# Performance work log

Measured on AMD Instinct MI355X. Metric: run time of the kernel, lower is better.

Reference implementation:

```python
import jax, jax.numpy as jnp
import numpy as np

N_NODES = 200000
N_EDGES = 3200000


def _gcn_prep(edge_index, n_nodes):
    # Add self loops (PyG GCNConv default) and compute symmetric normalization.
    loops = jnp.arange(n_nodes, dtype=edge_index.dtype)
    src = jnp.concatenate([edge_index[0], loops])
    dst = jnp.concatenate([edge_index[1], loops])
    deg = jax.ops.segment_sum(jnp.ones_like(dst, dtype=jnp.float32), dst,
                              num_segments=n_nodes)
    dinv = jnp.where(deg > 0, jax.lax.rsqrt(deg), 0.0)
    norm = dinv[src] * dinv[dst]  # [E+N]
    return src, dst, norm


def _gcn_conv(x, src, dst, norm, W, b, n_nodes):
    h = x @ W                                   # [N, out]
    msg = h[src] * norm[:, None]                # gather + scale, [E+N, out]
    out = jax.ops.segment_sum(msg, dst, num_segments=n_nodes)  # scatter-add
    return out + b


def setup_inputs() -> dict:
    key = jax.random.key(0)
    k = jax.random.split(key, 4)
    x = jax.random.normal(k[0], (N_NODES, 4), dtype=jnp.float32)
    edge_index = jax.random.randint(k[1], (2, N_EDGES), 0, N_NODES, dtype=jnp.int64)
    W1 = jax.random.normal(k[2], (4, 16), dtype=jnp.float32) * (1.0 / np.sqrt(4))
    b1 = jnp.zeros((16,), dtype=jnp.float32)
    W2 = jax.random.normal(k[3], (16, 1), dtype=jnp.float32) * (1.0 / np.sqrt(16))
    b2 = jnp.zeros((1,), dtype=jnp.float32)
    return {"x": x, "edge_index": edge_index, "W1": W1, "b1": b1,
            "W2": W2, "b2": b2}


def reference(x, edge_index, W1, b1, W2, b2):
    n = x.shape[0]
    src, dst, norm = _gcn_prep(edge_index, n)
    h = _gcn_conv(x, src, dst, norm, W1, b1, n)
    h = jax.nn.relu(h)
    out = _gcn_conv(h, src, dst, norm, W2, b2, n)
    return out
```

## Files before the change

### kernel.cpp

```cpp
#include <hip/hip_runtime.h>


#define BSE   512
#define CH    16384
#define NBW   512
#define SH    9
#define NB    391
#define FCAP  10752
#define BSB   512
#define RSTG  ((FCAP + BSB - 1) / BSB)
#define NOEDGE 0xFFFFFFFFu

__global__ void k_bin(const int* __restrict__ src, const int* __restrict__ dst,
                      int E, unsigned* __restrict__ gcur,
                      unsigned* __restrict__ epack) {
    __shared__ unsigned cnt[NB];
    __shared__ unsigned cur[NB];
    __shared__ unsigned basec[NB];
    int b = blockIdx.x, t = threadIdx.x;
    for (int i = t; i < NB; i += BSE) cnt[i] = 0;
    __syncthreads();
    int lo = b * CH, hi = min(E, lo + CH);
    int aligned = (hi - lo) & ~3;
    for (int i = lo + 4 * t; i + 3 < hi; i += 4 * BSE) {
        int4 d4 = *(const int4*)(dst + i);
        atomicAdd(&cnt[((unsigned)d4.x) >> SH], 1u);
        atomicAdd(&cnt[((unsigned)d4.y) >> SH], 1u);
        atomicAdd(&cnt[((unsigned)d4.z) >> SH], 1u);
        atomicAdd(&cnt[((unsigned)d4.w) >> SH], 1u);
    }
    for (int i = lo + aligned + t; i < hi; i += BSE)
        atomicAdd(&cnt[((unsigned)dst[i]) >> SH], 1u);
    __syncthreads();
    for (int i = t; i < NB; i += BSE) {
        unsigned c = cnt[i];
        unsigned pad = (c + 15u) & ~15u;
        unsigned ofs = pad ? atomicAdd(&gcur[i], pad) : 0u;
        unsigned base = (unsigned)i * FCAP + ofs;
        basec[i] = base;
        cur[i] = base;
    }
    __syncthreads();
    for (int i = lo + 4 * t; i + 3 < hi; i += 4 * BSE) {
        int4 d4 = *(const int4*)(dst + i);
        int4 s4 = *(const int4*)(src + i);
        unsigned k0 = ((unsigned)d4.x) >> SH, k1 = ((unsigned)d4.y) >> SH;
        unsigned k2 = ((unsigned)d4.z) >> SH, k3 = ((unsigned)d4.w) >> SH;
        unsigned p0 = atomicAdd(&cur[k0], 1u);
        unsigned p1 = atomicAdd(&cur[k1], 1u);
        unsigned p2 = atomicAdd(&cur[k2], 1u);
        unsigned p3 = atomicAdd(&cur[k3], 1u);
        if (p0 < (k0 + 1u) * FCAP) epack[p0] = ((unsigned)s4.x << SH) | (((unsigned)d4.x) & (NBW - 1u));
        if (p1 < (k1 + 1u) * FCAP) epack[p1] = ((unsigned)s4.y << SH) | (((unsigned)d4.y) & (NBW - 1u));
        if (p2 < (k2 + 1u) * FCAP) epack[p2] = ((unsigned)s4.z << SH) | (((unsigned)d4.z) & (NBW - 1u));
        if (p3 < (k3 + 1u) * FCAP) epack[p3] = ((unsigned)s4.w << SH) | (((unsigned)d4.w) & (NBW - 1u));
    }
    for (int i = lo + aligned + t; i < hi; i += BSE) {
        unsigned d = (unsigned)dst[i];
        unsigned k = d >> SH;
        unsigned pos = atomicAdd(&cur[k], 1u);
        if (pos < (k + 1u) * FCAP)
            epack[pos] = ((unsigned)src[i] << SH) | (d & (NBW - 1u));
    }
    __syncthreads();
    for (int i = t; i < NB; i += BSE) {
        unsigned end = basec[i] + ((cnt[i] + 15u) & ~15u);
        unsigned kend = ((unsigned)i + 1u) * FCAP;
        if (end > kend) end = kend;
        for (unsigned p = cur[i]; p < end; ++p) epack[p] = NOEDGE;
    }
}

__global__ void k_build(unsigned* __restrict__ epack, const unsigned* __restrict__ gcur,
                        const float* __restrict__ x,
                        unsigned* __restrict__ rowofs, unsigned* __restrict__ rowcnt,
                        float* __restrict__ x_scaled, int N) {
    __shared__ unsigned stage[FCAP];
    __shared__ unsigned cnt[BSB];
    __shared__ unsigned sc[BSB];
    __shared__ unsigned cur[BSB];
    int k = blockIdx.x, t = threadIdx.x;
    unsigned base = (unsigned)k * FCAP;
    int len = min((int)gcur[k], FCAP);
    for (int i = 4 * t; i + 3 < len; i += 4 * BSB)
        *(int4*)&stage[i] = *(const int4*)(epack + base + i);
    if (t < (len & 3)) stage[(len & ~3) + t] = epack[base + (len & ~3) + t];
    cnt[t] = 0;
    __syncthreads();
    for (int i = t; i < len; i += BSB) {
        unsigned p = stage[i];
        if (p != NOEDGE) atomicAdd(&cnt[p & (NBW - 1u)], 1u);
    }
    __syncthreads();
    unsigned c = cnt[t];
    sc[t] = c;
    __syncthreads();
    for (int off = 1; off < BSB; off <<= 1) {
        unsigned u = (t >= off) ? sc[t - off] : 0;
        __syncthreads();
        sc[t] += u;
        __syncthreads();
    }
    unsigned excl = sc[t] - c;
    cur[t] = excl;
    int node = k * NBW + t;
    if (node < N) {
        rowofs[node] = base + excl;
        rowcnt[node] = c;
        float di = rsqrtf((float)(c + 1));
        float4 xv = ((const float4*)x)[node];
        ((float4*)x_scaled)[node] = make_float4(xv.x * di, xv.y * di, xv.z * di, xv.w * di);
    }
    __syncthreads();
    int lenv = (int)sc[BSB - 1];
    unsigned r[RSTG];
    int nr = 0;
    for (int i = t; i < len; i += BSB) r[nr++] = stage[i];
    __syncthreads();
    for (int j = 0; j < nr; ++j) {
        unsigned p = r[j];
        if (p != NOEDGE) {
            unsigned pos = atomicAdd(&cur[p & (NBW - 1u)], 1u);
            stage[pos] = p >> SH;
        }
    }
    __syncthreads();
    for (int i = 4 * t; i + 3 < lenv; i += 4 * BSB)
        *(int4*)(epack + base + i) = *(const int4*)&stage[i];
    if (t < (lenv & 3)) epack[base + (lenv & ~3) + t] = stage[(lenv & ~3) + t];
}

__global__ void k_agg1(const unsigned* __restrict__ esorted, const unsigned* __restrict__ rowofs,
                       const unsigned* __restrict__ rowcnt,
                       const float* __restrict__ x_scaled,
                       const float* __restrict__ W1, const float* __restrict__ b1,
                       const float* __restrict__ W2,
                       float* __restrict__ z_scaled, int N) {
    int node = blockIdx.x * blockDim.x + threadIdx.x;
    if (node >= N) return;
    unsigned lo = rowofs[node], c = rowcnt[node], hi = lo + c;
    float di = rsqrtf((float)(c + 1));
    const float4* xs4 = (const float4*)x_scaled;
    float4 a0 = xs4[node];
    float4 a1 = make_float4(0.f, 0.f, 0.f, 0.f);
    float4 a2 = make_float4(0.f, 0.f, 0.f, 0.f);
    float4 a3 = make_float4(0.f, 0.f, 0.f, 0.f);
    unsigned i = lo;
    for (; i + 3 < hi; i += 4) {
        float4 v0 = xs4[esorted[i]],     v1 = xs4[esorted[i + 1]];
        float4 v2 = xs4[esorted[i + 2]], v3 = xs4[esorted[i + 3]];
        a0.x += v0.x; a0.y += v0.y; a0.z += v0.z; a0.w += v0.w;
        a1.x += v1.x; a1.y += v1.y; a1.z += v1.z; a1.w += v1.w;
        a2.x += v2.x; a2.y += v2.y; a2.z += v2.z; a2.w += v2.w;
        a3.x += v3.x; a3.y += v3.y; a3.z += v3.z; a3.w += v3.w;
    }
    for (; i < hi; ++i) {
        float4 v = xs4[esorted[i]];
        a0.x += v.x; a0.y += v.y; a0.z += v.z; a0.w += v.w;
    }
    float p0 = di * (a0.x + a1.x + a2.x + a3.x);
    float p1 = di * (a0.y + a1.y + a2.y + a3.y);
    float p2 = di * (a0.z + a1.z + a2.z + a3.z);
    float p3 = di * (a0.w + a1.w + a2.w + a3.w);
    float z = 0.0f;
    #pragma unroll
    for (int cc = 0; cc < 16; ++cc) {
        float h1 = p0 * W1[0 * 16 + cc] + p1 * W1[1 * 16 + cc]
                 + p2 * W1[2 * 16 + cc] + p3 * W1[3 * 16 + cc] + b1[cc];
        h1 = fmaxf(h1, 0.0f);
        z += h1 * W2[cc];
    }
    z_scaled[node] = z * di;
}

__global__ void k_agg2(const unsigned* __restrict__ esorted, const unsigned* __restrict__ rowofs,
                       const unsigned* __restrict__ rowcnt,
                       const float* __restrict__ z_scaled,
                       const float* __restrict__ b2, float* __restrict__ out, int N) {
    int node = blockIdx.x * blockDim.x + threadIdx.x;
    if (node >= N) return;
    unsigned lo = rowofs[node], c = rowcnt[node], hi = lo + c;
    float di = rsqrtf((float)(c + 1));
    float a0 = z_scaled[node], a1 = 0.f, a2 = 0.f, a3 = 0.f;
    unsigned i = lo;
    for (; i + 3 < hi; i += 4) {
        a0 += z_scaled[esorted[i]];
        a1 += z_scaled[esorted[i + 1]];
        a2 += z_scaled[esorted[i + 2]];
        a3 += z_scaled[esorted[i + 3]];
    }
    for (; i < hi; ++i) a0 += z_scaled[esorted[i]];
    out[node] = di * (a0 + a1 + a2 + a3) + b2[0];
}

extern "C" void kernel_launch(void* const* d_in, const int* in_sizes, int n_in,
                              void* d_out, int out_size, void* d_ws, size_t ws_size,
                              hipStream_t stream) {
    const float* x  = (const float*)d_in[0];
    const int*   ei = (const int*)d_in[1];
    const float* W1 = (const float*)d_in[2];
    const float* b1 = (const float*)d_in[3];
    const float* W2 = (const float*)d_in[4];
    const float* b2 = (const float*)d_in[5];

    const int N = in_sizes[0] / 4;
    const int E = in_sizes[1] / 2;
    const int* src = ei;
    const int* dst = ei + E;
    const int NA = (E + CH - 1) / CH;

    char* ws = (char*)d_ws;
    unsigned* gcur      = (unsigned*)ws;  ws += 4096;
    unsigned* epack     = (unsigned*)ws;  ws += (size_t)NB * FCAP * 4;
    unsigned* rowofs    = (unsigned*)ws;  ws += (size_t)N * 4;
    unsigned* rowcnt    = (unsigned*)ws;  ws += (size_t)N * 4;
    float*    x_scaled  = (float*)ws;     ws += (size_t)N * 4 * 4;
    float*    z_scaled  = (float*)ws;     ws += (size_t)N * 4;
    float* out = (float*)d_out;

    hipMemsetAsync(gcur, 0, NB * sizeof(unsigned), stream);
    k_bin  <<<NA, BSE, 0, stream>>>(src, dst, E, gcur, epack);
    k_build<<<NB, BSB, 0, stream>>>(epack, gcur, x, rowofs, rowcnt, x_scaled, N);
    k_agg1 <<<(N + 255) / 256, 256, 0, stream>>>(epack, rowofs, rowcnt, x_scaled,
                                                 W1, b1, W2, z_scaled, N);
    k_agg2 <<<(N + 255) / 256, 256, 0, stream>>>(epack, rowofs, rowcnt, z_scaled,
                                                 b2, out, N);
}
```

Before: 172.4 us.

## Fuse binning, CSR build and both aggregations into one cooperative kernel

Replaces the four kernel launches with a single cooperative kernel of one block per 512-node bucket, separated by grid syncs. The sorted edge list stays in shared memory, so the write-back of sorted indices and the rowofs/rowcnt arrays go away, and both aggregation passes read neighbor ids from LDS. The cost is a grid of only about 391 blocks, each with roughly 50KB of shared memory, doing the binning with smaller chunks, plus three grid-wide barriers. Degree-skewed buckets may leave blocks idle during aggregation.

```diff
diff --git a/kernel.cpp b/kernel.cpp
--- a/kernel.cpp
+++ b/kernel.cpp
@@ -1,167 +1,161 @@
 #include <hip/hip_runtime.h>
-
-
-#define BSE   512
-#define CH    16384
-#define NBW   512
-#define SH    9
-#define NB    391
-#define FCAP  10752
-#define BSB   512
-#define RSTG  ((FCAP + BSB - 1) / BSB)
+#include <hip/hip_cooperative_groups.h>
+
+namespace cg = cooperative_groups;
+
+#define BS     512
+#define NBW    512
+#define SH     9
+#define CH2    8192
+#define FCAP   12608
+#define RSTG   ((FCAP + BS - 1) / BS)
 #define NOEDGE 0xFFFFFFFFu
 
-__global__ void k_bin(const int* __restrict__ src, const int* __restrict__ dst,
-                      int E, unsigned* __restrict__ gcur,
-                      unsigned* __restrict__ epack) {
-    __shared__ unsigned cnt[NB];
-    __shared__ unsigned cur[NB];
-    __shared__ unsigned basec[NB];
-    int b = blockIdx.x, t = threadIdx.x;
-    for (int i = t; i < NB; i += BSE) cnt[i] = 0;
-    __syncthreads();
-    int lo = b * CH, hi = min(E, lo + CH);
-    int aligned = (hi - lo) & ~3;
-    for (int i = lo + 4 * t; i + 3 < hi; i += 4 * BSE) {
-        int4 d4 = *(const int4*)(dst + i);
-        atomicAdd(&cnt[((unsigned)d4.x) >> SH], 1u);
-        atomicAdd(&cnt[((unsigned)d4.y) >> SH], 1u);
-        atomicAdd(&cnt[((unsigned)d4.z) >> SH], 1u);
-        atomicAdd(&cnt[((unsigned)d4.w) >> SH], 1u);
-    }
-    for (int i = lo + aligned + t; i < hi; i += BSE)
-        atomicAdd(&cnt[((unsigned)dst[i]) >> SH], 1u);
-    __syncthreads();
-    for (int i = t; i < NB; i += BSE) {
-        unsigned c = cnt[i];
-        unsigned pad = (c + 15u) & ~15u;
-        unsigned ofs = pad ? atomicAdd(&gcur[i], pad) : 0u;
-        unsigned base = (unsigned)i * FCAP + ofs;
-        basec[i] = base;
-        cur[i] = base;
-    }
-    __syncthreads();
-    for (int i = lo + 4 * t; i + 3 < hi; i += 4 * BSE) {
-        int4 d4 = *(const int4*)(dst + i);
-        int4 s4 = *(const int4*)(src + i);
-        unsigned k0 = ((unsigned)d4.x) >> SH, k1 = ((unsigned)d4.y) >> SH;
-        unsigned k2 = ((unsigned)d4.z) >> SH, k3 = ((unsigned)d4.w) >> SH;
-        unsigned p0 = atomicAdd(&cur[k0], 1u);
-        unsigned p1 = atomicAdd(&cur[k1], 1u);
-        unsigned p2 = atomicAdd(&cur[k2], 1u);
-        unsigned p3 = atomicAdd(&cur[k3], 1u);
-        if (p0 < (k0 + 1u) * FCAP) epack[p0] = ((unsigned)s4.x << SH) | (((unsigned)d4.x) & (NBW - 1u));
-        if (p1 < (k1 + 1u) * FCAP) epack[p1] = ((unsigned)s4.y << SH) | (((unsigned)d4.y) & (NBW - 1u));
-        if (p2 < (k2 + 1u) * FCAP) epack[p2] = ((unsigned)s4.z << SH) | (((unsigned)d4.z) & (NBW - 1u));
-        if (p3 < (k3 + 1u) * FCAP) epack[p3] = ((unsigned)s4.w << SH) | (((unsigned)d4.w) & (NBW - 1u));
-    }
-    for (int i = lo + aligned + t; i < hi; i += BSE) {
-        unsigned d = (unsigned)dst[i];
-        unsigned k = d >> SH;
-        unsigned pos = atomicAdd(&cur[k], 1u);
-        if (pos < (k + 1u) * FCAP)
-            epack[pos] = ((unsigned)src[i] << SH) | (d & (NBW - 1u));
-    }
-    __syncthreads();
-    for (int i = t; i < NB; i += BSE) {
-        unsigned end = basec[i] + ((cnt[i] + 15u) & ~15u);
-        unsigned kend = ((unsigned)i + 1u) * FCAP;
-        if (end > kend) end = kend;
-        for (unsigned p = cur[i]; p < end; ++p) epack[p] = NOEDGE;
-    }
-}
-
-__global__ void k_build(unsigned* __restrict__ epack, const unsigned* __restrict__ gcur,
-                        const float* __restrict__ x,
-                        unsigned* __restrict__ rowofs, unsigned* __restrict__ rowcnt,
-                        float* __restrict__ x_scaled, int N) {
+__global__ __launch_bounds__(BS, 4)
+void k_fused(const int* __restrict__ src, const int* __restrict__ dst, int E,
+             unsigned* __restrict__ gcur, unsigned* __restrict__ epack,
+             const float* __restrict__ x,
+             const float* __restrict__ W1, const float* __restrict__ b1,
+             const float* __restrict__ W2, const float* __restrict__ b2,
+             float* __restrict__ x_scaled, float* __restrict__ z_scaled,
+             float* __restrict__ out, int N, int nb) {
     __shared__ unsigned stage[FCAP];
-    __shared__ unsigned cnt[BSB];
-    __shared__ unsigned sc[BSB];
-    __shared__ unsigned cur[BSB];
-    int k = blockIdx.x, t = threadIdx.x;
-    unsigned base = (unsigned)k * FCAP;
-    int len = min((int)gcur[k], FCAP);
-    for (int i = 4 * t; i + 3 < len; i += 4 * BSB)
+    __shared__ unsigned shA[BS];
+    __shared__ unsigned shB[BS];
+    __shared__ unsigned shC[BS];
+    cg::grid_group grid = cg::this_grid();
+    const int b = blockIdx.x, t = threadIdx.x;
+
+    for (int blk = b; blk * CH2 < E; blk += gridDim.x) {
+        for (int i = t; i < nb; i += BS) shA[i] = 0;
+        __syncthreads();
+        const int lo = blk * CH2, hi = min(E, lo + CH2);
+        const int aligned = (hi - lo) & ~3;
+        for (int i = lo + 4 * t; i + 3 < hi; i += 4 * BS) {
+            int4 d4 = *(const int4*)(dst + i);
+            atomicAdd(&shA[((unsigned)d4.x) >> SH], 1u);
+            atomicAdd(&shA[((unsigned)d4.y) >> SH], 1u);
+            atomicAdd(&shA[((unsigned)d4.z) >> SH], 1u);
+            atomicAdd(&shA[((unsigned)d4.w) >> SH], 1u);
+        }
+        for (int i = lo + aligned + t; i < hi; i += BS)
+            atomicAdd(&shA[((unsigned)dst[i]) >> SH], 1u);
+        __syncthreads();
+        for (int i = t; i < nb; i += BS) {
+            unsigned c   = shA[i];
+            unsigned pad = (c + 15u) & ~15u;
+            unsigned ofs = pad ? atomicAdd(&gcur[i], pad) : 0u;
+            unsigned bse = (unsigned)i * FCAP + ofs;
+            shC[i] = bse;
+            shB[i] = bse;
+        }
+        __syncthreads();
+        for (int i = lo + 4 * t; i + 3 < hi; i += 4 * BS) {
+            int4 d4 = *(const int4*)(dst + i);
+            int4 s4 = *(const int4*)(src + i);
+            unsigned k0 = ((unsigned)d4.x) >> SH, k1 = ((unsigned)d4.y) >> SH;
+            unsigned k2 = ((unsigned)d4.z) >> SH, k3 = ((unsigned)d4.w) >> SH;
+            unsigned p0 = atomicAdd(&shB[k0], 1u);
+            unsigned p1 = atomicAdd(&shB[k1], 1u);
+            unsigned p2 = atomicAdd(&shB[k2], 1u);
+            unsigned p3 = atomicAdd(&shB[k3], 1u);
+            if (p0 < (k0 + 1u) * FCAP) epack[p0] = ((unsigned)s4.x << SH) | (((unsigned)d4.x) & (NBW - 1u));
+            if (p1 < (k1 + 1u) * FCAP) epack[p1] = ((unsigned)s4.y << SH) | (((unsigned)d4.y) & (NBW - 1u));
+            if (p2 < (k2 + 1u) * FCAP) epack[p2] = ((unsigned)s4.z << SH) | (((unsigned)d4.z) & (NBW - 1u));
+            if (p3 < (k3 + 1u) * FCAP) epack[p3] = ((unsigned)s4.w << SH) | (((unsigned)d4.w) & (NBW - 1u));
+        }
+        for (int i = lo + aligned + t; i < hi; i += BS) {
+            unsigned d = (unsigned)dst[i];
+            unsigned k = d >> SH;
+            unsigned pos = atomicAdd(&shB[k], 1u);
+            if (pos < (k + 1u) * FCAP)
+                epack[pos] = ((unsigned)src[i] << SH) | (d & (NBW - 1u));
+        }
+        __syncthreads();
+        for (int i = t; i < nb; i += BS) {
+            unsigned end  = shC[i] + ((shA[i] + 15u) & ~15u);
+            unsigned kend = ((unsigned)i + 1u) * FCAP;
+            if (end > kend) end = kend;
+            for (unsigned p = shB[i]; p < end; ++p) epack[p] = NOEDGE;
+        }
+        __syncthreads();
+    }
+    grid.sync();
+
+    const unsigned base = (unsigned)b * FCAP;
+    const int len = min((int)gcur[b], FCAP);
+    for (int i = 4 * t; i + 3 < len; i += 4 * BS)
         *(int4*)&stage[i] = *(const int4*)(epack + base + i);
     if (t < (len & 3)) stage[(len & ~3) + t] = epack[base + (len & ~3) + t];
-    cnt[t] = 0;
-    __syncthreads();
-    for (int i = t; i < len; i += BSB) {
+    shA[t] = 0;
+    __syncthreads();
+    for (int i = t; i < len; i += BS) {
         unsigned p = stage[i];
-        if (p != NOEDGE) atomicAdd(&cnt[p & (NBW - 1u)], 1u);
-    }
-    __syncthreads();
-    unsigned c = cnt[t];
-    sc[t] = c;
-    __syncthreads();
-    for (int off = 1; off < BSB; off <<= 1) {
-        unsigned u = (t >= off) ? sc[t - off] : 0;
-        __syncthreads();
-        sc[t] += u;
-        __syncthreads();
-    }
-    unsigned excl = sc[t] - c;
-    cur[t] = excl;
-    int node = k * NBW + t;
+        if (p != NOEDGE) atomicAdd(&shA[p & (NBW - 1u)], 1u);
+    }
+    __syncthreads();
+    const unsigned c = shA[t];
+    shB[t] = c;
+    __syncthreads();
+    for (int off = 1; off < BS; off <<= 1) {
+        unsigned u = (t >= off) ? shB[t - off] : 0u;
+        __syncthreads();
+        shB[t] += u;
+        __syncthreads();
+    }
+    const unsigned excl = shB[t] - c;
+    shC[t] = excl;
+    const int node = b * NBW + t;
+    const float di = rsqrtf((float)(c + 1u));
+    float4 xs = make_float4(0.f, 0.f, 0.f, 0.f);
     if (node < N) {
-        rowofs[node] = base + excl;
-        rowcnt[node] = c;
-        float di = rsqrtf((float)(c + 1));
         float4 xv = ((const float4*)x)[node];
-        ((float4*)x_scaled)[node] = make_float4(xv.x * di, xv.y * di, xv.z * di, xv.w * di);
-    }
-    __syncthreads();
-    int lenv = (int)sc[BSB - 1];
+        xs = make_float4(xv.x * di, xv.y * di, xv.z * di, xv.w * di);
+        ((float4*)x_scaled)[node] = xs;
+    }
+    __syncthreads();
     unsigned r[RSTG];
-    int nr = 0;
-    for (int i = t; i < len; i += BSB) r[nr++] = stage[i];
-    __syncthreads();
-    for (int j = 0; j < nr; ++j) {
+    #pragma unroll
+    for (int j = 0; j < RSTG; ++j) {
+        int i = t + j * BS;
+        r[j] = (i < len) ? stage[i] : NOEDGE;
+    }
+    __syncthreads();
+    #pragma unroll
+    for (int j = 0; j < RSTG; ++j) {
         unsigned p = r[j];
         if (p != NOEDGE) {
-            unsigned pos = atomicAdd(&cur[p & (NBW - 1u)], 1u);
+            unsigned pos = atomicAdd(&shC[p & (NBW - 1u)], 1u);
             stage[pos] = p >> SH;
         }
     }
     __syncthreads();
-    for (int i = 4 * t; i + 3 < lenv; i += 4 * BSB)
-        *(int4*)(epack + base + i) = *(const int4*)&stage[i];
-    if (t < (lenv & 3)) epack[base + (lenv & ~3) + t] = stage[(lenv & ~3) + t];
-}
-
-__global__ void k_agg1(const unsigned* __restrict__ esorted, const unsigned* __restrict__ rowofs,
-                       const unsigned* __restrict__ rowcnt,
-                       const float* __restrict__ x_scaled,
-                       const float* __restrict__ W1, const float* __restrict__ b1,
-                       const float* __restrict__ W2,
-                       float* __restrict__ z_scaled, int N) {
-    int node = blockIdx.x * blockDim.x + threadIdx.x;
-    if (node >= N) return;
-    unsigned lo = rowofs[node], c = rowcnt[node], hi = lo + c;
-    float di = rsqrtf((float)(c + 1));
+    grid.sync();
+
     const float4* xs4 = (const float4*)x_scaled;
-    float4 a0 = xs4[node];
+    float4 a0 = xs;
     float4 a1 = make_float4(0.f, 0.f, 0.f, 0.f);
     float4 a2 = make_float4(0.f, 0.f, 0.f, 0.f);
     float4 a3 = make_float4(0.f, 0.f, 0.f, 0.f);
-    unsigned i = lo;
-    for (; i + 3 < hi; i += 4) {
-        float4 v0 = xs4[esorted[i]],     v1 = xs4[esorted[i + 1]];
-        float4 v2 = xs4[esorted[i + 2]], v3 = xs4[esorted[i + 3]];
-        a0.x += v0.x; a0.y += v0.y; a0.z += v0.z; a0.w += v0.w;
-        a1.x += v1.x; a1.y += v1.y; a1.z += v1.z; a1.w += v1.w;
-        a2.x += v2.x; a2.y += v2.y; a2.z += v2.z; a2.w += v2.w;
-        a3.x += v3.x; a3.y += v3.y; a3.z += v3.z; a3.w += v3.w;
-    }
-    for (; i < hi; ++i) {
-        float4 v = xs4[esorted[i]];
-        a0.x += v.x; a0.y += v.y; a0.z += v.z; a0.w += v.w;
-    }
-    float p0 = di * (a0.x + a1.x + a2.x + a3.x);
-    float p1 = di * (a0.y + a1.y + a2.y + a3.y);
-    float p2 = di * (a0.z + a1.z + a2.z + a3.z);
-    float p3 = di * (a0.w + a1.w + a2.w + a3.w);
+    {
+        unsigned i = excl, e = excl + c;
+        for (; i + 3 < e; i += 4) {
+            unsigned n0 = stage[i], n1 = stage[i + 1], n2 = stage[i + 2], n3 = stage[i + 3];
+            float4 v0 = xs4[n0], v1 = xs4[n1], v2 = xs4[n2], v3 = xs4[n3];
+            a0.x += v0.x; a0.y += v0.y; a0.z += v0.z; a0.w += v0.w;
+            a1.x += v1.x; a1.y += v1.y; a1.z += v1.z; a1.w += v1.w;
+            a2.x += v2.x; a2.y += v2.y; a2.z += v2.z; a2.w += v2.w;
+            a3.x += v3.x; a3.y += v3.y; a3.z += v3.z; a3.w += v3.w;
+        }
+        for (; i < e; ++i) {
+            float4 v = xs4[stage[i]];
+            a0.x += v.x; a0.y += v.y; a0.z += v.z; a0.w += v.w;
+        }
+    }
+    const float p0 = di * (a0.x + a1.x + a2.x + a3.x);
+    const float p1 = di * (a0.y + a1.y + a2.y + a3.y);
+    const float p2 = di * (a0.z + a1.z + a2.z + a3.z);
+    const float p3 = di * (a0.w + a1.w + a2.w + a3.w);
     float z = 0.0f;
     #pragma unroll
     for (int cc = 0; cc < 16; ++cc) {
@@ -170,27 +164,22 @@
         h1 = fmaxf(h1, 0.0f);
         z += h1 * W2[cc];
     }
-    z_scaled[node] = z * di;
-}
-
-__global__ void k_agg2(const unsigned* __restrict__ esorted, const unsigned* __restrict__ rowofs,
-                       const unsigned* __restrict__ rowcnt,
-                       const float* __restrict__ z_scaled,
-                       const float* __restrict__ b2, float* __restrict__ out, int N) {
-    int node = blockIdx.x * blockDim.x + threadIdx.x;
-    if (node >= N) return;
-    unsigned lo = rowofs[node], c = rowcnt[node], hi = lo + c;
-    float di = rsqrtf((float)(c + 1));
-    float a0 = z_scaled[node], a1 = 0.f, a2 = 0.f, a3 = 0.f;
-    unsigned i = lo;
-    for (; i + 3 < hi; i += 4) {
-        a0 += z_scaled[esorted[i]];
-        a1 += z_scaled[esorted[i + 1]];
-        a2 += z_scaled[esorted[i + 2]];
-        a3 += z_scaled[esorted[i + 3]];
-    }
-    for (; i < hi; ++i) a0 += z_scaled[esorted[i]];
-    out[node] = di * (a0 + a1 + a2 + a3) + b2[0];
+    const float zdi = z * di;
+    if (node < N) z_scaled[node] = zdi;
+    grid.sync();
+
+    float s0 = zdi, s1 = 0.f, s2 = 0.f, s3 = 0.f;
+    {
+        unsigned i = excl, e = excl + c;
+        for (; i + 3 < e; i += 4) {
+            s0 += z_scaled[stage[i]];
+            s1 += z_scaled[stage[i + 1]];
+            s2 += z_scaled[stage[i + 2]];
+            s3 += z_scaled[stage[i + 3]];
+        }
+        for (; i < e; ++i) s0 += z_scaled[stage[i]];
+    }
+    if (node < N) out[node] = di * (s0 + s1 + s2 + s3) + b2[0];
 }
 
 extern "C" void kernel_launch(void* const* d_in, const int* in_sizes, int n_in,
@@ -203,26 +192,25 @@
     const float* W2 = (const float*)d_in[4];
     const float* b2 = (const float*)d_in[5];
 
-    const int N = in_sizes[0] / 4;
-    const int E = in_sizes[1] / 2;
+    int N = in_sizes[0] / 4;
+    int E = in_sizes[1] / 2;
     const int* src = ei;
     const int* dst = ei + E;
-    const int NA = (E + CH - 1) / CH;
+    int nb = (N + NBW - 1) / NBW;
 
     char* ws = (char*)d_ws;
-    unsigned* gcur      = (unsigned*)ws;  ws += 4096;
-    unsigned* epack     = (unsigned*)ws;  ws += (size_t)NB * FCAP * 4;
-    unsigned* rowofs    = (unsigned*)ws;  ws += (size_t)N * 4;
-    unsigned* rowcnt    = (unsigned*)ws;  ws += (size_t)N * 4;
-    float*    x_scaled  = (float*)ws;     ws += (size_t)N * 4 * 4;
-    float*    z_scaled  = (float*)ws;     ws += (size_t)N * 4;
+    unsigned* gcur  = (unsigned*)ws;  ws += 4096;
+    unsigned* epack = (unsigned*)ws;  ws += (size_t)nb * FCAP * 4;
+    float* x_scaled = (float*)ws;     ws += (size_t)N * 4 * 4;
+    float* z_scaled = (float*)ws;     ws += (size_t)N * 4;
     float* out = (float*)d_out;
 
-    hipMemsetAsync(gcur, 0, NB * sizeof(unsigned), stream);
-    k_bin  <<<NA, BSE, 0, stream>>>(src, dst, E, gcur, epack);
-    k_build<<<NB, BSB, 0, stream>>>(epack, gcur, x, rowofs, rowcnt, x_scaled, N);
-    k_agg1 <<<(N + 255) / 256, 256, 0, stream>>>(epack, rowofs, rowcnt, x_scaled,
-                                                 W1, b1, W2, z_scaled, N);
-    k_agg2 <<<(N + 255) / 256, 256, 0, stream>>>(epack, rowofs, rowcnt, z_scaled,
-                                                 b2, out, N);
+    hipMemsetAsync(gcur, 0, nb * sizeof(unsigned), stream);
+
+    void* args[] = {
+        (void*)&src, (void*)&dst, (void*)&E, (void*)&gcur, (void*)&epack,
+        (void*)&x, (void*)&W1, (void*)&b1, (void*)&W2, (void*)&b2,
+        (void*)&x_scaled, (void*)&z_scaled, (void*)&out, (void*)&N, (void*)&nb
+    };
+    hipLaunchCooperativeKernel((void*)k_fused, dim3(nb), dim3(BS), args, 0, stream);
 }
```

Result: slower. 331.2 us (+92.1%).

## Pack row offset and count into one word, use wave-shuffle scan in build

Applied to the files above, without the earlier changes.

The build kernel now loads its bin straight into registers rather than staging through shared memory first. It replaces the 512-step shared-memory Hillis-Steele scan with a wave-level shuffle scan plus a small cross-wave scan, which removes many barriers. Per-node row offset and count are packed into a single 32-bit meta word, with the offset relative to the bin base and the count in the upper bits. This halves the per-node metadata reads in both aggregation kernels, at the cost of a few bit operations to rebuild the global offset. The packing assumes per-bin offsets fit in 14 bits and counts fit in 18 bits, which holds for FCAP of 10752.

```diff
diff --git a/kernel.cpp b/kernel.cpp
--- a/kernel.cpp
+++ b/kernel.cpp
@@ -73,51 +73,63 @@
 
 __global__ void k_build(unsigned* __restrict__ epack, const unsigned* __restrict__ gcur,
                         const float* __restrict__ x,
-                        unsigned* __restrict__ rowofs, unsigned* __restrict__ rowcnt,
+                        unsigned* __restrict__ meta,
                         float* __restrict__ x_scaled, int N) {
     __shared__ unsigned stage[FCAP];
     __shared__ unsigned cnt[BSB];
-    __shared__ unsigned sc[BSB];
     __shared__ unsigned cur[BSB];
-    int k = blockIdx.x, t = threadIdx.x;
-    unsigned base = (unsigned)k * FCAP;
-    int len = min((int)gcur[k], FCAP);
-    for (int i = 4 * t; i + 3 < len; i += 4 * BSB)
-        *(int4*)&stage[i] = *(const int4*)(epack + base + i);
-    if (t < (len & 3)) stage[(len & ~3) + t] = epack[base + (len & ~3) + t];
+    __shared__ unsigned wsum[BSB / 64];
+    __shared__ unsigned s_lenv;
+    const int k = blockIdx.x, t = threadIdx.x;
+    const unsigned base = (unsigned)k * FCAP;
+    const int len = min((int)gcur[k], FCAP);
+    unsigned r[RSTG];
+    #pragma unroll
+    for (int j = 0; j < RSTG; ++j) {
+        int i = t + j * BSB;
+        r[j] = (i < len) ? epack[base + i] : NOEDGE;
+    }
     cnt[t] = 0;
     __syncthreads();
-    for (int i = t; i < len; i += BSB) {
-        unsigned p = stage[i];
+    #pragma unroll
+    for (int j = 0; j < RSTG; ++j) {
+        unsigned p = r[j];
         if (p != NOEDGE) atomicAdd(&cnt[p & (NBW - 1u)], 1u);
     }
     __syncthreads();
-    unsigned c = cnt[t];
-    sc[t] = c;
-    __syncthreads();
-    for (int off = 1; off < BSB; off <<= 1) {
-        unsigned u = (t >= off) ? sc[t - off] : 0;
-        __syncthreads();
-        sc[t] += u;
-        __syncthreads();
-    }
-    unsigned excl = sc[t] - c;
+    const unsigned c = cnt[t];
+    unsigned v = c;
+    #pragma unroll
+    for (int off = 1; off < 64; off <<= 1) {
+        unsigned u = __shfl_up(v, off);
+        if ((t & 63) >= off) v += u;
+    }
+    if ((t & 63) == 63) wsum[t >> 6] = v;
+    __syncthreads();
+    if (t < BSB / 64) {
+        unsigned w = wsum[t];
+        #pragma unroll
+        for (int off = 1; off < BSB / 64; off <<= 1) {
+            unsigned u = __shfl_up(w, off);
+            if (t >= off) w += u;
+        }
+        wsum[t] = w;
+    }
+    __syncthreads();
+    const unsigned incl = v + ((t >> 6) ? wsum[(t >> 6) - 1] : 0u);
+    const unsigned excl = incl - c;
     cur[t] = excl;
-    int node = k * NBW + t;
+    if (t == BSB - 1) s_lenv = incl;
+    const int node = k * NBW + t;
     if (node < N) {
-        rowofs[node] = base + excl;
-        rowcnt[node] = c;
-        float di = rsqrtf((float)(c + 1));
+        meta[node] = excl | (c << 14);
+        float di = rsqrtf((float)(c + 1u));
         float4 xv = ((const float4*)x)[node];
         ((float4*)x_scaled)[node] = make_float4(xv.x * di, xv.y * di, xv.z * di, xv.w * di);
     }
     __syncthreads();
-    int lenv = (int)sc[BSB - 1];
-    unsigned r[RSTG];
-    int nr = 0;
-    for (int i = t; i < len; i += BSB) r[nr++] = stage[i];
-    __syncthreads();
-    for (int j = 0; j < nr; ++j) {
+    #pragma unroll
+    for (int j = 0; j < RSTG; ++j) {
         unsigned p = r[j];
         if (p != NOEDGE) {
             unsigned pos = atomicAdd(&cur[p & (NBW - 1u)], 1u);
@@ -125,21 +137,24 @@
         }
     }
     __syncthreads();
+    const int lenv = (int)s_lenv;
     for (int i = 4 * t; i + 3 < lenv; i += 4 * BSB)
         *(int4*)(epack + base + i) = *(const int4*)&stage[i];
     if (t < (lenv & 3)) epack[base + (lenv & ~3) + t] = stage[(lenv & ~3) + t];
 }
 
-__global__ void k_agg1(const unsigned* __restrict__ esorted, const unsigned* __restrict__ rowofs,
-                       const unsigned* __restrict__ rowcnt,
+__global__ void k_agg1(const unsigned* __restrict__ esorted, const unsigned* __restrict__ meta,
                        const float* __restrict__ x_scaled,
                        const float* __restrict__ W1, const float* __restrict__ b1,
                        const float* __restrict__ W2,
                        float* __restrict__ z_scaled, int N) {
     int node = blockIdx.x * blockDim.x + threadIdx.x;
     if (node >= N) return;
-    unsigned lo = rowofs[node], c = rowcnt[node], hi = lo + c;
-    float di = rsqrtf((float)(c + 1));
+    unsigned m = meta[node];
+    unsigned c = m >> 14;
+    unsigned lo = (unsigned)(node >> SH) * FCAP + (m & 16383u);
+    unsigned hi = lo + c;
+    float di = rsqrtf((float)(c + 1u));
     const float4* xs4 = (const float4*)x_scaled;
     float4 a0 = xs4[node];
     float4 a1 = make_float4(0.f, 0.f, 0.f, 0.f);
@@ -173,14 +188,16 @@
     z_scaled[node] = z * di;
 }
 
-__global__ void k_agg2(const unsigned* __restrict__ esorted, const unsigned* __restrict__ rowofs,
-                       const unsigned* __restrict__ rowcnt,
+__global__ void k_agg2(const unsigned* __restrict__ esorted, const unsigned* __restrict__ meta,
                        const float* __restrict__ z_scaled,
                        const float* __restrict__ b2, float* __restrict__ out, int N) {
     int node = blockIdx.x * blockDim.x + threadIdx.x;
     if (node >= N) return;
-    unsigned lo = rowofs[node], c = rowcnt[node], hi = lo + c;
-    float di = rsqrtf((float)(c + 1));
+    unsigned m = meta[node];
+    unsigned c = m >> 14;
+    unsigned lo = (unsigned)(node >> SH) * FCAP + (m & 16383u);
+    unsigned hi = lo + c;
+    float di = rsqrtf((float)(c + 1u));
     float a0 = z_scaled[node], a1 = 0.f, a2 = 0.f, a3 = 0.f;
     unsigned i = lo;
     for (; i + 3 < hi; i += 4) {
@@ -210,19 +227,17 @@
     const int NA = (E + CH - 1) / CH;
 
     char* ws = (char*)d_ws;
-    unsigned* gcur      = (unsigned*)ws;  ws += 4096;
-    unsigned* epack     = (unsigned*)ws;  ws += (size_t)NB * FCAP * 4;
-    unsigned* rowofs    = (unsigned*)ws;  ws += (size_t)N * 4;
-    unsigned* rowcnt    = (unsigned*)ws;  ws += (size_t)N * 4;
-    float*    x_scaled  = (float*)ws;     ws += (size_t)N * 4 * 4;
-    float*    z_scaled  = (float*)ws;     ws += (size_t)N * 4;
+    unsigned* gcur     = (unsigned*)ws;  ws += 4096;
+    unsigned* epack    = (unsigned*)ws;  ws += (size_t)NB * FCAP * 4;
+    unsigned* meta     = (unsigned*)ws;  ws += (size_t)N * 4;
+    float*    x_scaled = (float*)ws;     ws += (size_t)N * 4 * 4;
+    float*    z_scaled = (float*)ws;     ws += (size_t)N * 4;
     float* out = (float*)d_out;
 
     hipMemsetAsync(gcur, 0, NB * sizeof(unsigned), stream);
     k_bin  <<<NA, BSE, 0, stream>>>(src, dst, E, gcur, epack);
-    k_build<<<NB, BSB, 0, stream>>>(epack, gcur, x, rowofs, rowcnt, x_scaled, N);
-    k_agg1 <<<(N + 255) / 256, 256, 0, stream>>>(epack, rowofs, rowcnt, x_scaled,
+    k_build<<<NB, BSB, 0, stream>>>(epack, gcur, x, meta, x_scaled, N);
+    k_agg1 <<<(N + 255) / 256, 256, 0, stream>>>(epack, meta, x_scaled,
                                                  W1, b1, W2, z_scaled, N);
-    k_agg2 <<<(N + 255) / 256, 256, 0, stream>>>(epack, rowofs, rowcnt, z_scaled,
-                                                 b2, out, N);
-}
+    k_agg2 <<<(N + 255) / 256, 256, 0, stream>>>(epack, meta, z_scaled, b2, out, N);
+}
```

Measured after the change: 169.9 us. About the same (-1.5%).
